# Performance work log

Measured on AMD Instinct MI355X. Metric: run time of the kernel, lower is better.

The kernel has to match this reference:

```python
import jax, jax.numpy as jnp
import numpy as np

# Semantics of GPTQ Marlin 2:4 int4 GEMM: W_dense[K,N] has exactly 2 nonzeros per
# group of 4 along K. Compressed int4 values (q-8)*scale are stored packed 8-per-int32
# in B [K/16, N]; meta [K/4, N] in [0,6) selects which pair of the 4 positions is
# nonzero (index into the 6 combinations). s [K/groupsize, N] are group scales.

_PAIRS = jnp.array([[0, 1], [0, 2], [0, 3], [1, 2], [1, 3], [2, 3]], dtype=jnp.int32)


def _dequant_24(B, meta, s):
    Kd16, N = B.shape
    K = Kd16 * 16
    # unpack 8 nibbles per int32 -> [K/2, N] compressed values
    shifts = (jnp.arange(8, dtype=jnp.int32) * 4)[None, :, None]
    nib = (B[:, None, :] >> shifts) & 0xF            # [K/16, 8, N]
    vals = nib.reshape(K // 2, N).astype(jnp.float32) - 8.0  # symmetric zero-point 8
    gs = K // s.shape[0]                              # original groupsize
    scale = jnp.repeat(s, gs // 2, axis=0)            # [K/2, N] (compressed K dim)
    deq = (vals * scale).reshape(K // 4, 2, N)        # 2 values per group of 4
    pos = _PAIRS[meta]                                # [K/4, N, 2] positions in [0,4)
    oh = jax.nn.one_hot(pos, 4, dtype=jnp.float32)    # [K/4, N, 2, 4]
    W = jnp.einsum('gjn,gnjp->gpn', deq, oh)          # scatter into group slots
    return W.reshape(K, N)


def setup_inputs() -> dict:
    key = jax.random.key(0)
    k0, k1, k2, k3, k4 = jax.random.split(key, 5)
    M, K, N, GS = 8192, 4096, 4096, 128
    A = jax.random.normal(k0, (M, K), dtype=jnp.float32)
    B = jax.random.randint(k1, (K // 16, N), 0, 2147483647, dtype=jnp.int32)
    meta = jax.random.randint(k2, (K // 4, N), 0, 6, dtype=jnp.int32)
    s = jax.random.uniform(k3, (K // GS, N), dtype=jnp.float32, minval=0.005, maxval=0.02)
    bias = jax.random.normal(k4, (N,), dtype=jnp.float32)
    return {"A": A, "B": B, "meta": meta, "s": s, "bias": bias}


def reference(A, B, meta, s, bias):
    W = _dequant_24(B, meta, s)          # [K, N] dense 2:4-sparse dequantized weight
    return jnp.matmul(A, W, preferred_element_type=jnp.float32) + bias
```

## Files before the change

kernel.cpp:

```cpp
#include <hip/hip_runtime.h>

typedef _Float16 h16;
typedef __attribute__((ext_vector_type(8))) _Float16 h16x8;
typedef __attribute__((ext_vector_type(4))) float f32x4;
typedef unsigned int u32;

#define BARRIER() __builtin_amdgcn_s_barrier()
#define VMCNT(n)  asm volatile("s_waitcnt vmcnt(" #n ")" ::: "memory")

__global__ __launch_bounds__(256) void aux_kernel(const float* __restrict__ A,
    h16* __restrict__ Ah, int total8,
    const int* __restrict__ Bq, const int* __restrict__ meta,
    const float* __restrict__ s, h16* __restrict__ Wt,
    int K, int N, int chunksPerGroup, int nBlocksN) {
  const int bid = blockIdx.x;
  if (bid < 2048) {
    int stride = 2048 * 256;
    for (int i = bid * 256 + threadIdx.x; i < total8; i += stride) {
      const f32x4* p = (const f32x4*)(A + (size_t)i * 8);
      f32x4 v0 = p[0], v1 = p[1];
      h16x8 o;
      o[0] = (h16)v0[0]; o[1] = (h16)v0[1]; o[2] = (h16)v0[2]; o[3] = (h16)v0[3];
      o[4] = (h16)v1[0]; o[5] = (h16)v1[1]; o[6] = (h16)v1[2]; o[7] = (h16)v1[3];
      *(h16x8*)(Ah + (size_t)i * 8) = o;
    }
  } else {
    const int db = bid - 2048;
    const int n = (db % nBlocksN) * 256 + threadIdx.x;
    const int chunk = db / nBlocksN;
    u32 w0 = (u32)Bq[(size_t)(chunk * 2) * N + n];
    u32 w1 = (u32)Bq[(size_t)(chunk * 2 + 1) * N + n];
    float sc = s[(size_t)(chunk / chunksPerGroup) * N + n];
    h16 out[32];
#pragma unroll
    for (int gi = 0; gi < 8; ++gi) {
      int g = chunk * 8 + gi;
      int mm = meta[(size_t)g * N + n];
      u32 w = (gi < 4) ? w0 : w1;
      int j0 = (2 * gi) & 7;
      float d0 = (float)((int)((w >> (4 * j0)) & 0xFu) - 8) * sc;
      float d1 = (float)((int)((w >> (4 * j0 + 4)) & 0xFu) - 8) * sc;
      u32 enc = (0xED9C84u >> (4 * mm)) & 0xFu;
      int p0 = (int)(enc & 3u), p1 = (int)(enc >> 2);
#pragma unroll
      for (int p = 0; p < 4; ++p) {
        float v = (p == p0) ? d0 : ((p == p1) ? d1 : 0.0f);
        out[gi * 4 + p] = (h16)v;
      }
    }
    h16* dst = Wt + (size_t)n * K + chunk * 32;
    *(h16x8*)(dst + 0)  = *(h16x8*)(out + 0);
    *(h16x8*)(dst + 8)  = *(h16x8*)(out + 8);
    *(h16x8*)(dst + 16) = *(h16x8*)(out + 16);
    *(h16x8*)(dst + 24) = *(h16x8*)(out + 24);
  }
}

__global__ __launch_bounds__(1024, 4) void gemm_kernel(const h16* __restrict__ A,
    const h16* __restrict__ Wt, const float* __restrict__ bias,
    float* __restrict__ C, int M, int N, int K) {
  __shared__ alignas(16) h16 As[4][8192];
  __shared__ alignas(16) h16 Bs[4][8192];

  const int nTilesN = N >> 8;
  const int nwg = gridDim.x;
  int bid = blockIdx.x;
  int wg = (bid & 7) * (nwg >> 3) + (bid >> 3);
  int tm = wg / nTilesN, tn = wg - tm * nTilesN;

  const int t = threadIdx.x;
  const int lane = t & 63, w = t >> 6;
  const int wr = w >> 2, wc = w & 3;

  const int srow = t >> 2;
  const int chunk = (t & 3) ^ ((srow >> 1) & 3);
  const h16* gA_t = A + ((size_t)(tm * 256) + srow) * K + chunk * 8;
  const h16* gB_t = Wt + ((size_t)(tn * 256) + srow) * K + chunk * 8;
  const int t8 = t * 8;

#define GLOAD(SRC, DST) __builtin_amdgcn_global_load_lds(                      \
    (const __attribute__((address_space(1))) void*)(SRC),                      \
    (__attribute__((address_space(3))) void*)(DST), 16, 0, 0)

#define STAGE(T_) do {                                                         \
    GLOAD(gA_t + (size_t)(T_) * 32, &As[(T_) & 3][t8]);                        \
    GLOAD(gB_t + (size_t)(T_) * 32, &Bs[(T_) & 3][t8]);                        \
  } while (0)

  const int ln15 = lane & 15, l16 = lane >> 4;
  const int slA = (l16 ^ ((ln15 >> 1) & 3)) * 8;
  const int aBase = (wr * 64 + ln15) * 32 + slA;
  const int bBase = (wc * 64 + ln15) * 32 + slA;

  f32x4 acc[4][4] = {};
  const int NT = K >> 5;

  STAGE(0); STAGE(1); STAGE(2);
  VMCNT(4);
  BARRIER();

  for (int T = 0; T < NT; ++T) {
    const h16* aS = As[T & 3];
    const h16* bS = Bs[T & 3];
    h16x8 af[4], bf[4];
#pragma unroll
    for (int m = 0; m < 4; ++m) af[m] = *(const h16x8*)(aS + aBase + m * 512);
#pragma unroll
    for (int n = 0; n < 4; ++n) bf[n] = *(const h16x8*)(bS + bBase + n * 512);
    if (T + 3 < NT) STAGE(T + 3);
#pragma unroll
    for (int m = 0; m < 4; ++m)
#pragma unroll
      for (int n = 0; n < 4; ++n)
        acc[m][n] = __builtin_amdgcn_mfma_f32_16x16x32_f16(af[m], bf[n], acc[m][n], 0, 0, 0);
    if (T + 3 < NT) {
      VMCNT(4);
    } else if (T + 2 < NT) {
      VMCNT(2);
    } else if (T + 1 < NT) {
      VMCNT(0);
    }
    BARRIER();
  }

  int colBase = tn * 256 + wc * 64 + ln15;
  int rowBase = tm * 256 + wr * 64 + l16 * 4;
#pragma unroll
  for (int n = 0; n < 4; ++n) {
    float bv = bias[colBase + n * 16];
#pragma unroll
    for (int m = 0; m < 4; ++m) {
#pragma unroll
      for (int j = 0; j < 4; ++j) {
        C[(size_t)(rowBase + m * 16 + j) * N + colBase + n * 16] = acc[m][n][j] + bv;
      }
    }
  }
#undef STAGE
#undef GLOAD
}

extern "C" void kernel_launch(void* const* d_in, const int* in_sizes, int n_in,
                              void* d_out, int out_size, void* d_ws, size_t ws_size,
                              hipStream_t stream) {
  const float* A = (const float*)d_in[0];
  const int* Bq = (const int*)d_in[1];
  const int* meta = (const int*)d_in[2];
  const float* s = (const float*)d_in[3];
  const float* bias = (const float*)d_in[4];
  float* C = (float*)d_out;

  const int N = in_sizes[4];
  const int K = (int)(((long long)in_sizes[1] * 16) / N);
  const int M = (int)((long long)in_sizes[0] / K);
  const int sRows = (int)((long long)in_sizes[3] / N);
  const int chunksPerGroup = (K / sRows) / 32;
  const int nBlocksN = N / 256;

  h16* Ah = (h16*)d_ws;
  h16* Wt = Ah + (size_t)M * K;

  int auxGrid = 2048 + nBlocksN * (K / 32);
  aux_kernel<<<auxGrid, 256, 0, stream>>>(A, Ah, (M * K) / 8, Bq, meta, s, Wt,
                                          K, N, chunksPerGroup, nBlocksN);

  int grid = (M / 256) * (N / 256);
  gemm_kernel<<<grid, 1024, 0, stream>>>(Ah, Wt, bias, C, M, N, K);
}
```

Measured before the change: 283.0 us.

## Process two K-tiles per barrier with paired prefetch and full vmcnt drain

Restructures the GEMM main loop to compute two 32-wide K tiles per iteration. At the top of each iteration it issues loads for the next two tiles, then waits for all outstanding loads (vmcnt 0) and a single barrier. This halves the number of barriers per K, but the prefetch distance shrinks from three tiles to about one pair, so global-load latency may be less hidden behind compute. LDS ring buffers of 4 stages are reused, with tiles T+2/T+3 written into slots not being read.

```diff
diff --git a/kernel.cpp b/kernel.cpp
--- a/kernel.cpp
+++ b/kernel.cpp
@@ -95,31 +95,32 @@
   f32x4 acc[4][4] = {};
   const int NT = K >> 5;
 
-  STAGE(0); STAGE(1); STAGE(2);
-  VMCNT(4);
+#define TILE_BODY(T_) do {                                                     \
+    const h16* aS = As[(T_) & 3];                                              \
+    const h16* bS = Bs[(T_) & 3];                                              \
+    h16x8 af[4], bf[4];                                                        \
+    _Pragma("unroll")                                                          \
+    for (int m = 0; m < 4; ++m) af[m] = *(const h16x8*)(aS + aBase + m * 512); \
+    _Pragma("unroll")                                                          \
+    for (int n = 0; n < 4; ++n) bf[n] = *(const h16x8*)(bS + bBase + n * 512); \
+    _Pragma("unroll")                                                          \
+    for (int m = 0; m < 4; ++m)                                                \
+      _Pragma("unroll")                                                        \
+      for (int n = 0; n < 4; ++n)                                              \
+        acc[m][n] = __builtin_amdgcn_mfma_f32_16x16x32_f16(af[m], bf[n],       \
+                                                           acc[m][n], 0, 0, 0);\
+  } while (0)
+
+  STAGE(0); STAGE(1);
+  VMCNT(0);
   BARRIER();
 
-  for (int T = 0; T < NT; ++T) {
-    const h16* aS = As[T & 3];
-    const h16* bS = Bs[T & 3];
-    h16x8 af[4], bf[4];
-#pragma unroll
-    for (int m = 0; m < 4; ++m) af[m] = *(const h16x8*)(aS + aBase + m * 512);
-#pragma unroll
-    for (int n = 0; n < 4; ++n) bf[n] = *(const h16x8*)(bS + bBase + n * 512);
+  for (int T = 0; T < NT; T += 2) {
+    if (T + 2 < NT) STAGE(T + 2);
     if (T + 3 < NT) STAGE(T + 3);
-#pragma unroll
-    for (int m = 0; m < 4; ++m)
-#pragma unroll
-      for (int n = 0; n < 4; ++n)
-        acc[m][n] = __builtin_amdgcn_mfma_f32_16x16x32_f16(af[m], bf[n], acc[m][n], 0, 0, 0);
-    if (T + 3 < NT) {
-      VMCNT(4);
-    } else if (T + 2 < NT) {
-      VMCNT(2);
-    } else if (T + 1 < NT) {
-      VMCNT(0);
-    }
+    TILE_BODY(T);
+    TILE_BODY(T + 1);
+    VMCNT(0);
     BARRIER();
   }
 
@@ -136,6 +137,7 @@
       }
     }
   }
+#undef TILE_BODY
 #undef STAGE
 #undef GLOAD
 }
```

New measurement: 294.7 us. 1.04x slower.

## Prefetch next K-tile LDS fragments into registers during MFMAs

Applied to the files above, without the earlier changes.

Restructures the GEMM main loop so half of the A/B fragments for the next K-tile are read from LDS while the current tile's MFMAs run. Each iteration's 16 MFMAs are interleaved with the remaining LDS reads. The global-load wait is tightened so tile T+1 is resident one iteration earlier, and the barriers on the final iterations are dropped. This aims to hide LDS read latency behind matrix math, at the cost of extra live registers and a more fragile synchronisation schedule.

```diff
diff --git a/kernel.cpp b/kernel.cpp
--- a/kernel.cpp
+++ b/kernel.cpp
@@ -92,35 +92,48 @@
   const int aBase = (wr * 64 + ln15) * 32 + slA;
   const int bBase = (wc * 64 + ln15) * 32 + slA;
 
+#define MFMA1(M_, N_, AF_, BF_)                                                \
+  acc[M_][N_] = __builtin_amdgcn_mfma_f32_16x16x32_f16(AF_, BF_, acc[M_][N_], 0, 0, 0)
+
   f32x4 acc[4][4] = {};
   const int NT = K >> 5;
 
   STAGE(0); STAGE(1); STAGE(2);
-  VMCNT(4);
+  VMCNT(2);
   BARRIER();
+  h16x8 pA0 = *(const h16x8*)(As[0] + aBase);
+  h16x8 pA1 = *(const h16x8*)(As[0] + aBase + 512);
+  h16x8 pB0 = *(const h16x8*)(Bs[0] + bBase);
+  h16x8 pB1 = *(const h16x8*)(Bs[0] + bBase + 512);
 
   for (int T = 0; T < NT; ++T) {
     const h16* aS = As[T & 3];
     const h16* bS = Bs[T & 3];
-    h16x8 af[4], bf[4];
-#pragma unroll
-    for (int m = 0; m < 4; ++m) af[m] = *(const h16x8*)(aS + aBase + m * 512);
-#pragma unroll
-    for (int n = 0; n < 4; ++n) bf[n] = *(const h16x8*)(bS + bBase + n * 512);
+    const h16* aSn = As[(T + 1) & 3];
+    const h16* bSn = Bs[(T + 1) & 3];
     if (T + 3 < NT) STAGE(T + 3);
-#pragma unroll
-    for (int m = 0; m < 4; ++m)
-#pragma unroll
-      for (int n = 0; n < 4; ++n)
-        acc[m][n] = __builtin_amdgcn_mfma_f32_16x16x32_f16(af[m], bf[n], acc[m][n], 0, 0, 0);
+    h16x8 a2 = *(const h16x8*)(aS + aBase + 2 * 512);
+    h16x8 a3 = *(const h16x8*)(aS + aBase + 3 * 512);
+    h16x8 b2 = *(const h16x8*)(bS + bBase + 2 * 512);
+    h16x8 b3 = *(const h16x8*)(bS + bBase + 3 * 512);
+    MFMA1(0, 0, pA0, pB0); MFMA1(0, 1, pA0, pB1);
+    MFMA1(1, 0, pA1, pB0); MFMA1(1, 1, pA1, pB1);
+    MFMA1(2, 0, a2,  pB0); MFMA1(2, 1, a2,  pB1);
+    MFMA1(3, 0, a3,  pB0); MFMA1(3, 1, a3,  pB1);
+    pB0 = *(const h16x8*)(bSn + bBase);
+    pB1 = *(const h16x8*)(bSn + bBase + 512);
+    MFMA1(0, 2, pA0, b2); MFMA1(0, 3, pA0, b3);
+    MFMA1(1, 2, pA1, b2); MFMA1(1, 3, pA1, b3);
+    pA0 = *(const h16x8*)(aSn + aBase);
+    pA1 = *(const h16x8*)(aSn + aBase + 512);
+    MFMA1(2, 2, a2, b2); MFMA1(2, 3, a2, b3);
+    MFMA1(3, 2, a3, b2); MFMA1(3, 3, a3, b3);
     if (T + 3 < NT) {
-      VMCNT(4);
+      VMCNT(2);
     } else if (T + 2 < NT) {
-      VMCNT(2);
-    } else if (T + 1 < NT) {
       VMCNT(0);
     }
-    BARRIER();
+    if (T + 2 < NT) BARRIER();
   }
 
   int colBase = tn * 256 + wc * 64 + ln15;
@@ -136,6 +149,7 @@
       }
     }
   }
+#undef MFMA1
 #undef STAGE
 #undef GLOAD
 }
```

Result: slower. 336.6 us (+18.9%).
